# Kernel tuning notes

Measured on AMD Instinct MI355X. Metric: run time of the kernel, lower is better.

The kernel has to match this reference:

```python
import jax, jax.numpy as jnp
import numpy as np

B, S, E, H = 2, 2048, 1024, 16
D = E // H  # head_dim = 64


def setup_inputs() -> dict:
    key = jax.random.key(0)
    ks = jax.random.split(key, 9)
    s = 1.0 / np.sqrt(E)
    return {
        "x": jax.random.normal(ks[0], (B, S, E), dtype=jnp.float32),
        "Wq": jax.random.uniform(ks[1], (E, E), jnp.float32, -s, s),
        "bq": jax.random.uniform(ks[2], (E,), jnp.float32, -s, s),
        "Wk": jax.random.uniform(ks[3], (E, E), jnp.float32, -s, s),
        "bk": jax.random.uniform(ks[4], (E,), jnp.float32, -s, s),
        "Wv": jax.random.uniform(ks[5], (E, E), jnp.float32, -s, s),
        "bv": jax.random.uniform(ks[6], (E,), jnp.float32, -s, s),
        "Wo": jax.random.uniform(ks[7], (E, E), jnp.float32, -s, s),
        "bo": jax.random.uniform(ks[8], (E,), jnp.float32, -s, s),
    }


def reference(x, Wq, bq, Wk, bk, Wv, bv, Wo, bo):
    # QKV projections (torch Linear: x @ W.T + b), split into heads: [B,H,S,D]
    def proj(t, W, b):
        return (t @ W.T + b).reshape(B, S, H, D).transpose(0, 2, 1, 3)

    Q = proj(x, Wq, bq)
    K = proj(x, Wk, bk)
    V = proj(x, Wv, bv)
    # scores [B,H,S,S], scaled by sqrt(head_dim)
    score = jnp.einsum('bnqd,bnkd->bnqk', Q, K) / jnp.sqrt(jnp.float32(D))
    weights = jax.nn.softmax(score, axis=-1)
    out = jnp.einsum('bnql,bnld->bnqd', weights, V)  # [B,H,S,D]
    out = out.transpose(0, 2, 1, 3).reshape(B, S, E)
    return out @ Wo.T + bo
```

## Files before the change

kernel.cpp:

```cpp
#include <hip/hip_runtime.h>


#define B_ 2
#define S_ 2048
#define E_ 1024
#define H_ 16
#define D_ 64
#define M_ (B_ * S_)

typedef __attribute__((ext_vector_type(8))) _Float16 f16x8;
typedef __attribute__((ext_vector_type(4))) _Float16 f16x4;
typedef __attribute__((ext_vector_type(2))) _Float16 f16x2;
typedef __attribute__((ext_vector_type(4))) float f32x4;
typedef __attribute__((ext_vector_type(8))) unsigned short u16x8;

#define LOG2E  1.44269504f
#define CLOG2  4.32808512f

static __device__ __forceinline__ float bf16_to_f32(unsigned short u) {
    return __uint_as_float(((unsigned)u) << 16);
}
static __device__ __forceinline__ unsigned short f32_to_bf16(float f) {
    unsigned u = __float_as_uint(f);
    u += 0x7FFFu + ((u >> 16) & 1u);
    return (unsigned short)(u >> 16);
}
static __device__ __forceinline__ float load1_f32(const void* p, int i, bool isbf) {
    return isbf ? bf16_to_f32(((const unsigned short*)p)[i]) : ((const float*)p)[i];
}
static __device__ __forceinline__ void store1(void* p, size_t i, float v, bool isbf) {
    if (isbf) ((unsigned short*)p)[i] = f32_to_bf16(v);
    else      ((float*)p)[i] = v;
}
static __device__ __forceinline__ void gl2lds16(const void* g, void* l) {
    __builtin_amdgcn_global_load_lds((const __attribute__((address_space(1))) unsigned int*)g,
                                     (__attribute__((address_space(3))) unsigned int*)l, 16, 0, 0);
}
static __device__ __forceinline__ float rexp2(float x) {
    float r;
    asm("v_exp_f32 %0, %1" : "=v"(r) : "v"(x));
    return r;
}
static __device__ __forceinline__ f16x4 pack4(float e0, float e1, float e2, float e3) {
    f16x2 lo = __builtin_bit_cast(f16x2, __builtin_amdgcn_cvt_pkrtz(e0, e1));
    f16x2 hi = __builtin_bit_cast(f16x2, __builtin_amdgcn_cvt_pkrtz(e2, e3));
    return __builtin_shufflevector(lo, hi, 0, 1, 2, 3);
}

__global__ __launch_bounds__(256) void convert_inputs(
    const void* __restrict__ x,  const void* __restrict__ wq,
    const void* __restrict__ wk, const void* __restrict__ wv,
    const void* __restrict__ wo,
    _Float16* __restrict__ x16, _Float16* __restrict__ w16,
    int* __restrict__ flag_out)
{
    __shared__ int sflag;
    const int tid = threadIdx.x;
    if (tid < 64) {
        const unsigned short hh = ((const unsigned short*)x)[2 * tid];
        const int e = (hh >> 7) & 0xFF;
        const bool sane = (e >= 0x60 && e <= 0x9F);
        const unsigned long long m = __ballot(sane);
        if (tid == 0) sflag = (__popcll(m) >= 48) ? 1 : 0;
    }
    __syncthreads();
    const bool isbf = sflag != 0;
    if (blockIdx.x == 0 && tid == 0) *flag_out = sflag;

    const size_t t = ((size_t)blockIdx.x * 256 + tid) * 8;
    const void* src; size_t off; _Float16* dst; float scale = 1.0f;
    if (t < (size_t)M_ * E_) { src = x; off = t; dst = x16 + t; }
    else {
        const size_t u = t - (size_t)M_ * E_;
        const int wsel = (int)(u >> 20);
        off = u & ((1u << 20) - 1);
        src = wsel == 0 ? wq : wsel == 1 ? wk : wsel == 2 ? wv : wo;
        dst = w16 + u;
        if (wsel == 0) scale = 0.125f * LOG2E;
    }
    f16x8 v;
    if (isbf) {
        u16x8 s = *(const u16x8*)((const unsigned short*)src + off);
        #pragma unroll
        for (int j = 0; j < 8; ++j) v[j] = (_Float16)(bf16_to_f32(s[j]) * scale);
    } else {
        const float* f = (const float*)src + off;
        f32x4 lo = *(const f32x4*)f;
        f32x4 hi = *(const f32x4*)(f + 4);
        #pragma unroll
        for (int j = 0; j < 4; ++j) {
            v[j]     = (_Float16)(lo[j] * scale);
            v[4 + j] = (_Float16)(hi[j] * scale);
        }
    }
    *(f16x8*)dst = v;
}

__global__ __launch_bounds__(256) void gemm_qkv(
    const _Float16* __restrict__ x16, const _Float16* __restrict__ w16,
    const void* __restrict__ bq, const void* __restrict__ bk, const void* __restrict__ bv,
    const int* __restrict__ flag,
    _Float16* __restrict__ Qb, _Float16* __restrict__ Kb, _Float16* __restrict__ VTb)
{
    __shared__ __align__(16) _Float16 As[128 * 64];
    __shared__ __align__(16) _Float16 Bs[128 * 64];
    const bool isbf = (*flag != 0);
    const int tid = threadIdx.x, wave = tid >> 6, lane = tid & 63;
    const int wm = wave >> 1, wn = wave & 1;
    const int qd = lane >> 4, ln = lane & 15;
    const int m0 = blockIdx.x * 128;
    const int by = blockIdx.y;
    const int wsel = by >> 3;
    const int n0 = (by & 7) * 128;
    const _Float16* W = w16 + ((size_t)wsel << 20);

    char* dX = (wsel == 2) ? (char*)Bs : (char*)As;
    char* dW = (wsel == 2) ? (char*)As : (char*)Bs;

    const _Float16* gx[4]; const _Float16* gw[4];
    char* lx[4]; char* lw[4];
    #pragma unroll
    for (int it = 0; it < 4; ++it) {
        const int seg = it * 256 + tid;
        const int row = seg >> 3, cg = seg & 7;
        const int scol = ((cg + row) & 7) * 8;
        gx[it] = x16 + (size_t)(m0 + row) * E_ + scol;
        gw[it] = W + (size_t)(n0 + row) * E_ + scol;
        lx[it] = dX + (size_t)(it * 256 + wave * 64) * 16;
        lw[it] = dW + (size_t)(it * 256 + wave * 64) * 16;
    }

    const int sw0 = ((qd - ln) & 7) * 8;
    const int sw1 = ((qd + 4 - ln) & 7) * 8;

    f32x4 acc[16] = {};

    for (int kt = 0; kt < E_; kt += 64) {
        __syncthreads();
        #pragma unroll
        for (int it = 0; it < 4; ++it) {
            gl2lds16(gx[it] + kt, lx[it]);
            gl2lds16(gw[it] + kt, lw[it]);
        }
        __syncthreads();
        #pragma unroll
        for (int kk = 0; kk < 2; ++kk) {
            const int sw = kk ? sw1 : sw0;
            f16x8 a[4], bfr[4];
            #pragma unroll
            for (int mt = 0; mt < 4; ++mt)
                a[mt] = *(const f16x8*)&As[((wm * 64 + mt * 16 + ln) << 6) + sw];
            #pragma unroll
            for (int nt = 0; nt < 4; ++nt)
                bfr[nt] = *(const f16x8*)&Bs[((wn * 64 + nt * 16 + ln) << 6) + sw];
            #pragma unroll
            for (int mt = 0; mt < 4; ++mt)
                #pragma unroll
                for (int nt = 0; nt < 4; ++nt)
                    acc[mt * 4 + nt] = __builtin_amdgcn_mfma_f32_16x16x32_f16(a[mt], bfr[nt], acc[mt * 4 + nt], 0, 0, 0);
        }
    }

    if (wsel != 2) {
        const void* bias = wsel == 0 ? bq : bk;
        const float bscale = (wsel == 0) ? 0.125f * LOG2E : 1.0f;
        _Float16* dst = wsel == 0 ? Qb : Kb;
        #pragma unroll
        for (int nt = 0; nt < 4; ++nt) {
            const int n = n0 + wn * 64 + nt * 16 + ln;
            const float bvv = load1_f32(bias, n, isbf) * bscale;
            const int h = n >> 6, d = n & 63;
            #pragma unroll
            for (int mt = 0; mt < 4; ++mt)
                #pragma unroll
                for (int r = 0; r < 4; ++r) {
                    const int m = m0 + wm * 64 + mt * 16 + qd * 4 + r;
                    const int b = m >> 11, s = m & (S_ - 1);
                    dst[((size_t)(b * H_ + h) * S_ + s) * D_ + d] =
                        (_Float16)(acc[mt * 4 + nt][r] + bvv);
                }
        }
    } else {
        #pragma unroll
        for (int mt = 0; mt < 4; ++mt)
            #pragma unroll
            for (int r = 0; r < 4; ++r) {
                const int e = n0 + wm * 64 + mt * 16 + qd * 4 + r;
                const float bvv = load1_f32(bv, e, isbf);
                const int h = e >> 6, d = e & 63;
                #pragma unroll
                for (int nt = 0; nt < 4; ++nt) {
                    const int sg = m0 + wn * 64 + nt * 16 + ln;
                    const int b = sg >> 11, s = sg & (S_ - 1);
                    VTb[((size_t)(b * H_ + h) * D_ + d) * S_ + s] =
                        (_Float16)(acc[mt * 4 + nt][r] + bvv);
                }
            }
    }
}

__global__ __launch_bounds__(256, 4) void attn(
    const _Float16* __restrict__ Q, const _Float16* __restrict__ K,
    const _Float16* __restrict__ VT, _Float16* __restrict__ AO)
{
    __shared__ __align__(16) _Float16 Ks[2][64][64];
    __shared__ __align__(16) _Float16 Vs[2][64][64];
    __shared__ __align__(16) _Float16 Ps[64][64];

    const int tid = threadIdx.x, wave = tid >> 6, lane = tid & 63;
    const int qd = lane >> 4, ln = lane & 15;
    const int L = blockIdx.x;
    const int bh = ((L & 7) << 2) | ((L >> 3) & 3);
    const int qt = L >> 5;
    const int b = bh >> 4, h = bh & (H_ - 1);

    const _Float16* Kbase = K + (size_t)bh * S_ * D_;
    const _Float16* Vbase = VT + (size_t)bh * D_ * S_;

    f16x8 qf[2];
    {
        const _Float16* qrow = Q + ((size_t)bh * S_ + qt * 64 + wave * 16 + ln) * D_;
        qf[0] = *(const f16x8*)(qrow + qd * 8);
        qf[1] = *(const f16x8*)(qrow + 32 + qd * 8);
    }

    f16x8 ones;
    #pragma unroll
    for (int j = 0; j < 8; ++j) ones[j] = (_Float16)1.0f;

    const _Float16* kg[2]; const _Float16* vg[2]; int ldo[2];
    #pragma unroll
    for (int it = 0; it < 2; ++it) {
        const int seg = it * 256 + tid;
        const int row = seg >> 3, cg = seg & 7;
        const int scol = ((cg ^ (row & 7)) << 3);
        kg[it] = Kbase + (size_t)row * D_ + scol;
        vg[it] = Vbase + (size_t)row * S_ + scol;
        ldo[it] = (it * 256 + wave * 64) * 16;
    }

    const int swz0 = (qd * 16) ^ ((ln & 7) << 4);
    const int swz1 = (64 + qd * 16) ^ ((ln & 7) << 4);
    const int prow = (wave * 16 + ln) << 7;

    f32x4 o[4] = {};
    f32x4 li2 = {};

    #pragma unroll
    for (int it = 0; it < 2; ++it) {
        gl2lds16(kg[it], (char*)&Ks[0][0][0] + ldo[it]);
        gl2lds16(vg[it], (char*)&Vs[0][0][0] + ldo[it]);
    }
    __syncthreads();

    for (int kt = 0; kt < S_; kt += 64) {
        const int p = (kt >> 6) & 1;
        if (kt + 64 < S_) {
            const int np = p ^ 1;
            #pragma unroll
            for (int it = 0; it < 2; ++it) {
                gl2lds16(kg[it] + (size_t)(kt + 64) * D_, (char*)&Ks[np][0][0] + ldo[it]);
                gl2lds16(vg[it] + (kt + 64),              (char*)&Vs[np][0][0] + ldo[it]);
            }
        }

        const char* kb = (const char*)&Ks[p][0][0];
        const char* vb = (const char*)&Vs[p][0][0];

        f16x8 af[2][4], vf[2][4];
        #pragma unroll
        for (int kk = 0; kk < 2; ++kk) {
            const int swz = kk ? swz1 : swz0;
            #pragma unroll
            for (int t4 = 0; t4 < 4; ++t4) {
                af[kk][t4] = *(const f16x8*)(kb + ((t4 * 16 + ln) << 7) + swz);
                vf[kk][t4] = *(const f16x8*)(vb + ((t4 * 16 + ln) << 7) + swz);
            }
        }

        f32x4 sc[4] = {};
        __builtin_amdgcn_s_setprio(1);
        #pragma unroll
        for (int kk = 0; kk < 2; ++kk)
            #pragma unroll
            for (int t4 = 0; t4 < 4; ++t4)
                sc[t4] = __builtin_amdgcn_mfma_f32_16x16x32_f16(af[kk][t4], qf[kk], sc[t4], 0, 0, 0);
        __builtin_amdgcn_s_setprio(0);

        #pragma unroll
        for (int t4 = 0; t4 < 4; ++t4) {
            f16x4 ph = pack4(rexp2(sc[t4][0] - CLOG2), rexp2(sc[t4][1] - CLOG2),
                             rexp2(sc[t4][2] - CLOG2), rexp2(sc[t4][3] - CLOG2));
            *(f16x4*)((char*)&Ps[0][0] + prow + ((t4 * 32 + qd * 8) ^ ((ln & 7) << 4))) = ph;
        }

        #pragma unroll
        for (int kk = 0; kk < 2; ++kk) {
            f16x8 pf = *(const f16x8*)((const char*)&Ps[0][0] + prow + (kk ? swz1 : swz0));
            __builtin_amdgcn_s_setprio(1);
            #pragma unroll
            for (int dt = 0; dt < 4; ++dt)
                o[dt] = __builtin_amdgcn_mfma_f32_16x16x32_f16(pf, vf[kk][dt], o[dt], 0, 0, 0);
            li2 = __builtin_amdgcn_mfma_f32_16x16x32_f16(pf, ones, li2, 0, 0, 0);
            __builtin_amdgcn_s_setprio(0);
        }

        __syncthreads();
    }

    #pragma unroll
    for (int r = 0; r < 4; ++r) {
        const float inv = 1.0f / li2[r];
        const int s = qt * 64 + wave * 16 + qd * 4 + r;
        #pragma unroll
        for (int dt = 0; dt < 4; ++dt)
            AO[((size_t)b * S_ + s) * E_ + h * D_ + dt * 16 + ln] = (_Float16)(o[dt][r] * inv);
    }
}

__global__ __launch_bounds__(256) void gemm_out(
    const _Float16* __restrict__ A, const _Float16* __restrict__ W,
    const void* __restrict__ bias, const int* __restrict__ flag, void* __restrict__ out)
{
    __shared__ __align__(16) _Float16 As[128 * 64];
    __shared__ __align__(16) _Float16 Bs[128 * 64];
    const bool isbf = (*flag != 0);
    const int tid = threadIdx.x, wave = tid >> 6, lane = tid & 63;
    const int wm = wave >> 1, wn = wave & 1;
    const int qd = lane >> 4, ln = lane & 15;
    const int m0 = blockIdx.x * 128;
    const int n0 = blockIdx.y * 128;

    const _Float16* ga[4]; const _Float16* gb[4];
    char* la[4]; char* lb[4];
    #pragma unroll
    for (int it = 0; it < 4; ++it) {
        const int seg = it * 256 + tid;
        const int row = seg >> 3, cg = seg & 7;
        const int scol = ((cg + row) & 7) * 8;
        ga[it] = A + (size_t)(m0 + row) * E_ + scol;
        gb[it] = W + (size_t)(n0 + row) * E_ + scol;
        la[it] = (char*)As + (size_t)(it * 256 + wave * 64) * 16;
        lb[it] = (char*)Bs + (size_t)(it * 256 + wave * 64) * 16;
    }
    const int sw0 = ((qd - ln) & 7) * 8;
    const int sw1 = ((qd + 4 - ln) & 7) * 8;

    f32x4 acc[16] = {};

    for (int kt = 0; kt < E_; kt += 64) {
        __syncthreads();
        #pragma unroll
        for (int it = 0; it < 4; ++it) {
            gl2lds16(ga[it] + kt, la[it]);
            gl2lds16(gb[it] + kt, lb[it]);
        }
        __syncthreads();
        #pragma unroll
        for (int kk = 0; kk < 2; ++kk) {
            const int sw = kk ? sw1 : sw0;
            f16x8 a[4], bfr[4];
            #pragma unroll
            for (int mt = 0; mt < 4; ++mt)
                a[mt] = *(const f16x8*)&As[((wm * 64 + mt * 16 + ln) << 6) + sw];
            #pragma unroll
            for (int nt = 0; nt < 4; ++nt)
                bfr[nt] = *(const f16x8*)&Bs[((wn * 64 + nt * 16 + ln) << 6) + sw];
            #pragma unroll
            for (int mt = 0; mt < 4; ++mt)
                #pragma unroll
                for (int nt = 0; nt < 4; ++nt)
                    acc[mt * 4 + nt] = __builtin_amdgcn_mfma_f32_16x16x32_f16(a[mt], bfr[nt], acc[mt * 4 + nt], 0, 0, 0);
        }
    }

    #pragma unroll
    for (int nt = 0; nt < 4; ++nt) {
        const int n = n0 + wn * 64 + nt * 16 + ln;
        const float bvv = load1_f32(bias, n, isbf);
        #pragma unroll
        for (int mt = 0; mt < 4; ++mt)
            #pragma unroll
            for (int r = 0; r < 4; ++r) {
                const int m = m0 + wm * 64 + mt * 16 + qd * 4 + r;
                store1(out, (size_t)m * E_ + n, acc[mt * 4 + nt][r] + bvv, isbf);
            }
    }
}

extern "C" void kernel_launch(void* const* d_in, const int* in_sizes, int n_in,
                              void* d_out, int out_size, void* d_ws, size_t ws_size,
                              hipStream_t stream) {
    const void* x  = d_in[0];
    const void* Wq = d_in[1];
    const void* bq = d_in[2];
    const void* Wk = d_in[3];
    const void* bk = d_in[4];
    const void* Wv = d_in[5];
    const void* bv = d_in[6];
    const void* Wo = d_in[7];
    const void* bo = d_in[8];

    int* flag = (int*)d_ws;
    _Float16* x16 = (_Float16*)((char*)d_ws + 1024);
    _Float16* w16 = x16 + (size_t)M_ * E_;
    _Float16* Qb  = w16 + 4u * (size_t)E_ * E_;
    _Float16* Kb  = Qb + (size_t)M_ * E_;
    _Float16* VTb = Kb + (size_t)M_ * E_;
    _Float16* AO  = x16;

    convert_inputs<<<4096, 256, 0, stream>>>(x, Wq, Wk, Wv, Wo, x16, w16, flag);
    gemm_qkv<<<dim3(32, 24), 256, 0, stream>>>(x16, w16, bq, bk, bv, flag, Qb, Kb, VTb);
    attn<<<1024, 256, 0, stream>>>(Qb, Kb, VTb, AO);
    gemm_out<<<dim3(32, 8), 256, 0, stream>>>(AO, w16 + 3u * (size_t)E_ * E_, bo, flag, d_out);
}
```

Measured before the change: 208.3 us.

## Rework attention inner loop with 32x32 MFMA and split-K across waves

The attention kernel now uses 32x32x16 MFMA tiles. Waves are split into two query groups times two key halves, and the two key halves are reduced through shared memory at the end. The S-to-P exponentials are packed straight into the B-operand registers instead of going through a shared-memory P tile, which removes the Ps buffer and its writes and reads. In exchange it adds a final cross-wave reduction and narrower f16x4 loads of V. It also changes register pressure with larger accumulators.

```diff
diff --git a/kernel.cpp b/kernel.cpp
--- a/kernel.cpp
+++ b/kernel.cpp
@@ -12,7 +12,9 @@
 typedef __attribute__((ext_vector_type(4))) _Float16 f16x4;
 typedef __attribute__((ext_vector_type(2))) _Float16 f16x2;
 typedef __attribute__((ext_vector_type(4))) float f32x4;
+typedef __attribute__((ext_vector_type(16))) float f32x16;
 typedef __attribute__((ext_vector_type(8))) unsigned short u16x8;
+typedef __attribute__((ext_vector_type(4))) unsigned int u32x4;
 
 #define LOG2E  1.44269504f
 #define CLOG2  4.32808512f
@@ -41,10 +43,8 @@
     asm("v_exp_f32 %0, %1" : "=v"(r) : "v"(x));
     return r;
 }
-static __device__ __forceinline__ f16x4 pack4(float e0, float e1, float e2, float e3) {
-    f16x2 lo = __builtin_bit_cast(f16x2, __builtin_amdgcn_cvt_pkrtz(e0, e1));
-    f16x2 hi = __builtin_bit_cast(f16x2, __builtin_amdgcn_cvt_pkrtz(e2, e3));
-    return __builtin_shufflevector(lo, hi, 0, 1, 2, 3);
+static __device__ __forceinline__ unsigned pk2(float a, float b) {
+    return __builtin_bit_cast(unsigned, __builtin_amdgcn_cvt_pkrtz(a, b));
 }
 
 __global__ __launch_bounds__(256) void convert_inputs(
@@ -203,25 +203,26 @@
     const _Float16* __restrict__ Q, const _Float16* __restrict__ K,
     const _Float16* __restrict__ VT, _Float16* __restrict__ AO)
 {
-    __shared__ __align__(16) _Float16 Ks[2][64][64];
-    __shared__ __align__(16) _Float16 Vs[2][64][64];
-    __shared__ __align__(16) _Float16 Ps[64][64];
+    __shared__ __align__(16) char smem[32768];
+    _Float16* Ksb = (_Float16*)smem;
+    _Float16* Vsb = (_Float16*)(smem + 16384);
 
     const int tid = threadIdx.x, wave = tid >> 6, lane = tid & 63;
-    const int qd = lane >> 4, ln = lane & 15;
+    const int rl = lane & 31, h = lane >> 5, r7 = rl & 7;
+    const int qg = wave & 1, kh = wave >> 1;
     const int L = blockIdx.x;
     const int bh = ((L & 7) << 2) | ((L >> 3) & 3);
     const int qt = L >> 5;
-    const int b = bh >> 4, h = bh & (H_ - 1);
+    const int b = bh >> 4, hh = bh & (H_ - 1);
 
     const _Float16* Kbase = K + (size_t)bh * S_ * D_;
     const _Float16* Vbase = VT + (size_t)bh * D_ * S_;
 
-    f16x8 qf[2];
+    f16x8 qf[4];
     {
-        const _Float16* qrow = Q + ((size_t)bh * S_ + qt * 64 + wave * 16 + ln) * D_;
-        qf[0] = *(const f16x8*)(qrow + qd * 8);
-        qf[1] = *(const f16x8*)(qrow + 32 + qd * 8);
+        const _Float16* qrow = Q + ((size_t)bh * S_ + qt * 64 + qg * 32 + rl) * D_ + h * 8;
+        #pragma unroll
+        for (int c = 0; c < 4; ++c) qf[c] = *(const f16x8*)(qrow + c * 16);
     }
 
     f16x8 ones;
@@ -239,17 +240,19 @@
         ldo[it] = (it * 256 + wave * 64) * 16;
     }
 
-    const int swz0 = (qd * 16) ^ ((ln & 7) << 4);
-    const int swz1 = (64 + qd * 16) ^ ((ln & 7) << 4);
-    const int prow = (wave * 16 + ln) << 7;
-
-    f32x4 o[4] = {};
-    f32x4 li2 = {};
+    int koff[4];
+    #pragma unroll
+    for (int c = 0; c < 4; ++c)
+        koff[c] = ((kh * 32 + rl) << 7) + ((((c << 1) | h) ^ r7) << 4);
+    const int vrow0 = rl << 7, vrow1 = (32 + rl) << 7;
+    const int hb = h << 3;
+
+    f32x16 o0 = {}, o1 = {}, li = {};
 
     #pragma unroll
     for (int it = 0; it < 2; ++it) {
-        gl2lds16(kg[it], (char*)&Ks[0][0][0] + ldo[it]);
-        gl2lds16(vg[it], (char*)&Vs[0][0][0] + ldo[it]);
+        gl2lds16(kg[it], (char*)Ksb + ldo[it]);
+        gl2lds16(vg[it], (char*)Vsb + ldo[it]);
     }
     __syncthreads();
 
@@ -259,62 +262,78 @@
             const int np = p ^ 1;
             #pragma unroll
             for (int it = 0; it < 2; ++it) {
-                gl2lds16(kg[it] + (size_t)(kt + 64) * D_, (char*)&Ks[np][0][0] + ldo[it]);
-                gl2lds16(vg[it] + (kt + 64),              (char*)&Vs[np][0][0] + ldo[it]);
+                gl2lds16(kg[it] + (size_t)(kt + 64) * D_, (char*)Ksb + np * 8192 + ldo[it]);
+                gl2lds16(vg[it] + (kt + 64),              (char*)Vsb + np * 8192 + ldo[it]);
             }
         }
 
-        const char* kb = (const char*)&Ks[p][0][0];
-        const char* vb = (const char*)&Vs[p][0][0];
-
-        f16x8 af[2][4], vf[2][4];
-        #pragma unroll
-        for (int kk = 0; kk < 2; ++kk) {
-            const int swz = kk ? swz1 : swz0;
-            #pragma unroll
-            for (int t4 = 0; t4 < 4; ++t4) {
-                af[kk][t4] = *(const f16x8*)(kb + ((t4 * 16 + ln) << 7) + swz);
-                vf[kk][t4] = *(const f16x8*)(vb + ((t4 * 16 + ln) << 7) + swz);
-            }
-        }
-
-        f32x4 sc[4] = {};
+        const char* kb = (const char*)Ksb + p * 8192;
+        const char* vb = (const char*)Vsb + p * 8192;
+
+        f16x8 af[4];
+        #pragma unroll
+        for (int c = 0; c < 4; ++c) af[c] = *(const f16x8*)(kb + koff[c]);
+
+        f32x16 sc = {};
         __builtin_amdgcn_s_setprio(1);
         #pragma unroll
-        for (int kk = 0; kk < 2; ++kk)
-            #pragma unroll
-            for (int t4 = 0; t4 < 4; ++t4)
-                sc[t4] = __builtin_amdgcn_mfma_f32_16x16x32_f16(af[kk][t4], qf[kk], sc[t4], 0, 0, 0);
+        for (int c = 0; c < 4; ++c)
+            sc = __builtin_amdgcn_mfma_f32_32x32x16_f16(af[c], qf[c], sc, 0, 0, 0);
         __builtin_amdgcn_s_setprio(0);
 
-        #pragma unroll
-        for (int t4 = 0; t4 < 4; ++t4) {
-            f16x4 ph = pack4(rexp2(sc[t4][0] - CLOG2), rexp2(sc[t4][1] - CLOG2),
-                             rexp2(sc[t4][2] - CLOG2), rexp2(sc[t4][3] - CLOG2));
-            *(f16x4*)((char*)&Ps[0][0] + prow + ((t4 * 32 + qd * 8) ^ ((ln & 7) << 4))) = ph;
-        }
-
-        #pragma unroll
-        for (int kk = 0; kk < 2; ++kk) {
-            f16x8 pf = *(const f16x8*)((const char*)&Ps[0][0] + prow + (kk ? swz1 : swz0));
+        float e[16];
+        #pragma unroll
+        for (int i = 0; i < 16; ++i) e[i] = rexp2(sc[i] - CLOG2);
+
+        #pragma unroll
+        for (int ks = 0; ks < 2; ++ks) {
+            const int oo = 8 * ks;
+            const f16x8 pf = __builtin_bit_cast(f16x8, (u32x4){
+                pk2(e[oo + 0], e[oo + 1]), pk2(e[oo + 2], e[oo + 3]),
+                pk2(e[oo + 4], e[oo + 5]), pk2(e[oo + 6], e[oo + 7])});
+
+            const int cA = ((((kh << 2) | (ks << 1)) ^ r7) << 4) + hb;
+            const int cB = ((((kh << 2) | (ks << 1) | 1) ^ r7) << 4) + hb;
+            const f16x4 a0 = *(const f16x4*)(vb + vrow0 + cA);
+            const f16x4 b0 = *(const f16x4*)(vb + vrow0 + cB);
+            const f16x4 a1 = *(const f16x4*)(vb + vrow1 + cA);
+            const f16x4 b1 = *(const f16x4*)(vb + vrow1 + cB);
+            const f16x8 v0 = __builtin_shufflevector(a0, b0, 0, 1, 2, 3, 4, 5, 6, 7);
+            const f16x8 v1 = __builtin_shufflevector(a1, b1, 0, 1, 2, 3, 4, 5, 6, 7);
+
             __builtin_amdgcn_s_setprio(1);
-            #pragma unroll
-            for (int dt = 0; dt < 4; ++dt)
-                o[dt] = __builtin_amdgcn_mfma_f32_16x16x32_f16(pf, vf[kk][dt], o[dt], 0, 0, 0);
-            li2 = __builtin_amdgcn_mfma_f32_16x16x32_f16(pf, ones, li2, 0, 0, 0);
+            o0 = __builtin_amdgcn_mfma_f32_32x32x16_f16(pf, v0, o0, 0, 0, 0);
+            o1 = __builtin_amdgcn_mfma_f32_32x32x16_f16(pf, v1, o1, 0, 0, 0);
+            li = __builtin_amdgcn_mfma_f32_32x32x16_f16(pf, ones, li, 0, 0, 0);
             __builtin_amdgcn_s_setprio(0);
         }
 
         __syncthreads();
     }
 
-    #pragma unroll
-    for (int r = 0; r < 4; ++r) {
-        const float inv = 1.0f / li2[r];
-        const int s = qt * 64 + wave * 16 + qd * 4 + r;
-        #pragma unroll
-        for (int dt = 0; dt < 4; ++dt)
-            AO[((size_t)b * S_ + s) * E_ + h * D_ + dt * 16 + ln] = (_Float16)(o[dt][r] * inv);
+    float* red = (float*)smem;
+    const int rbase = qg * 64 + lane;
+    if (kh) {
+        #pragma unroll
+        for (int i = 0; i < 16; ++i) {
+            red[i * 128 + rbase]        = o0[i];
+            red[(16 + i) * 128 + rbase] = o1[i];
+            red[(32 + i) * 128 + rbase] = li[i];
+        }
+    }
+    __syncthreads();
+    if (!kh) {
+        #pragma unroll
+        for (int i = 0; i < 16; ++i) {
+            const float t0 = o0[i] + red[i * 128 + rbase];
+            const float t1 = o1[i] + red[(16 + i) * 128 + rbase];
+            const float tl = li[i] + red[(32 + i) * 128 + rbase];
+            const float inv = 1.0f / tl;
+            const int q = qt * 64 + qg * 32 + 4 * h + (i & 3) + 8 * (i >> 2);
+            _Float16* dst = AO + ((size_t)b * S_ + q) * E_ + hh * D_;
+            dst[rl]      = (_Float16)(t0 * inv);
+            dst[32 + rl] = (_Float16)(t1 * inv);
+        }
     }
 }
 
```

After: 207.2 us. Within noise of the previous version (-0.5%).
